# Optimization experiments

Hardware: AMD Instinct MI355X
Metric: run time of the kernel (lower is better)

## Reference

```python
import jax, jax.numpy as jnp
import numpy as np

N = 100000      # total nodes in batched graph
E_RAND = 1600000  # random edges (avg degree 16); self-loops appended -> E = E_RAND + N
B = 1024        # number of graphs / descriptor batch
DIN, D2D, D3D = 128, 200, 100
DG, DH = 20, 64
H1, H2 = 128, 32
EPS = 1e-5


def _lin_init(key, fan_in, fan_out):
    k1, k2 = jax.random.split(key)
    bound = 1.0 / np.sqrt(fan_in)
    W = jax.random.uniform(k1, (fan_in, fan_out), jnp.float32, -bound, bound)
    b = jax.random.uniform(k2, (fan_out,), jnp.float32, -bound, bound)
    return W, b


def setup_inputs() -> dict:
    key = jax.random.key(0)
    ks = jax.random.split(key, 16)
    feat = jax.random.normal(ks[0], (N, DIN), jnp.float32)
    src_r = jax.random.randint(ks[1], (E_RAND,), 0, N, jnp.int32)
    dst_r = jax.random.randint(ks[2], (E_RAND,), 0, N, jnp.int32)
    loop = jnp.arange(N, dtype=jnp.int32)
    src = jnp.concatenate([src_r, loop])  # self-loops: every node has in-degree >= 1
    dst = jnp.concatenate([dst_r, loop])
    graph_id = ((jnp.arange(N, dtype=jnp.int64) * B) // N).astype(jnp.int32)  # sorted, all B nonempty
    desc_2d = jax.random.normal(ks[3], (B, D2D), jnp.float32)
    desc_3d = jax.random.normal(ks[4], (B, D3D), jnp.float32)
    Wg1, bg1 = _lin_init(ks[5], DIN, 100)
    Wg2, bg2 = _lin_init(ks[6], 100, DG)
    Wpg, bpg = _lin_init(ks[7], DG, DH)
    Wp2, bp2 = _lin_init(ks[8], D2D, DH)
    gain = np.sqrt(6.0 / (DH + DH))
    W2 = jax.random.uniform(ks[9], (DH, DH), jnp.float32, -gain, gain)  # xavier_uniform
    Wf1, bf1 = _lin_init(ks[10], 2 * DH, H1)
    Wf2, bf2 = _lin_init(ks[11], H1, H2)
    Wf3, bf3 = _lin_init(ks[12], H2, 1)
    return dict(feat=feat, src=src, dst=dst, graph_id=graph_id,
                desc_2d=desc_2d, desc_3d=desc_3d,
                Wg1=Wg1, bg1=bg1, Wg2=Wg2, bg2=bg2,
                Wpg=Wpg, bpg=bpg, Wp2=Wp2, bp2=bp2, W2=W2,
                Wf1=Wf1, bf1=bf1, Wf2=Wf2, bf2=bf2, Wf3=Wf3, bf3=bf3,
                bn1_g=jnp.ones((H1,), jnp.float32), bn1_b=jnp.zeros((H1,), jnp.float32),
                bn2_g=jnp.ones((H2,), jnp.float32), bn2_b=jnp.zeros((H2,), jnp.float32))


def _gcn(h, W, b, src, dst):
    # copy_u -> mailbox mean: segment-mean of source feats over destination
    msg = h[src]                                               # [E, d] gather
    s = jax.ops.segment_sum(msg, dst, num_segments=N)          # [N, d]
    deg = jax.ops.segment_sum(jnp.ones((src.shape[0], 1), h.dtype), dst, num_segments=N)
    accum = s / jnp.maximum(deg, 1.0)
    return jax.nn.relu(accum @ W + b)


def _bn(x, g, b):  # BatchNorm1d, training-mode batch stats (biased var)
    mu = jnp.mean(x, axis=0)
    var = jnp.mean(jnp.square(x - mu), axis=0)
    return g * (x - mu) * jax.lax.rsqrt(var + EPS) + b


def reference(feat, src, dst, graph_id, desc_2d, desc_3d,
              Wg1, bg1, Wg2, bg2, Wpg, bpg, Wp2, bp2, W2,
              Wf1, bf1, Wf2, bf2, Wf3, bf3, bn1_g, bn1_b, bn2_g, bn2_b):
    h = _gcn(feat, Wg1, bg1, src, dst)        # relu(GCN1) -> [N,100]
    h = _gcn(h, Wg2, bg2, src, dst)           # relu(GCN2) -> [N,20]
    # dgl.mean_nodes: per-graph mean
    hs = jax.ops.segment_sum(h, graph_id, num_segments=B)
    cnt = jax.ops.segment_sum(jnp.ones((N, 1), h.dtype), graph_id, num_segments=B)
    hg = hs / jnp.maximum(cnt, 1.0)           # [B, 20]
    h_g = hg @ Wpg + bpg                      # [B, 64]
    h_d = desc_2d @ Wp2 + bp2                 # [B, 64]
    gate_vec = jax.nn.sigmoid((h_g @ W2) * h_d)
    v2 = gate_vec * h_d
    fusion = jnp.concatenate([h_g, v2], axis=-1)   # [B, 128]
    out = jax.nn.relu(_bn(fusion @ Wf1 + bf1, bn1_g, bn1_b))
    out = jax.nn.relu(_bn(out @ Wf2 + bf2, bn2_g, bn2_b))
    return out @ Wf3 + bf3                    # [B, 1]
```

## Files before the change

### kernel.cpp

```cpp
#include <hip/hip_runtime.h>
#include <hip/hip_fp8.h>
#include <math.h>

#define N_NODES 100000
#define B_GRAPH 1024
#define NBKT 391
#define NBLK 416
#define CAP 6000

typedef unsigned short ushort_t;
typedef unsigned int uint_t;
typedef unsigned char uchar_t;
typedef __attribute__((ext_vector_type(8))) short short8v;
typedef __attribute__((ext_vector_type(4))) float f32x4;
typedef __attribute__((ext_vector_type(2))) float f32x2;

static inline size_t alignup(size_t x){ return (x + 255) & ~(size_t)255; }

__device__ inline float bflo(uint_t u){
  union{ uint_t i; float f; } v; v.i = u << 16; return v.f;
}
__device__ inline float bfhi(uint_t u){
  union{ uint_t i; float f; } v; v.i = u & 0xffff0000u; return v.f;
}
__device__ inline ushort_t f2bf(float f){
  union{ float f; uint_t i; } v; v.f = f;
  uint_t b = v.i;
  b += 0x7fffu + ((b >> 16) & 1u);
  return (ushort_t)(b >> 16);
}
__device__ inline uint_t packbf(float a, float b){
  return (uint_t)f2bf(a) | ((uint_t)f2bf(b) << 16);
}
__device__ inline uchar_t f2fp8(float f){
  __hip_fp8_e4m3 v(f); return (uchar_t)v.__x;
}

__global__ __launch_bounds__(256) void k_hist(const int* __restrict__ dst,
                                              int* __restrict__ hist_g, int* __restrict__ btot,
                                              int E, int CH){
  __shared__ int h[NBKT];
  int blk = blockIdx.x, t = threadIdx.x;
  for (int i = t; i < NBKT; i += 256) h[i] = 0;
  __syncthreads();
  int s = blk*CH, e = s + CH; if (e > E) e = E;
  for (int i = s + t; i < e; i += 256) atomicAdd(&h[dst[i] >> 8], 1);
  __syncthreads();
  for (int i = t; i < NBKT; i += 256){
    int v = h[i];
    hist_g[i*NBLK + blk] = v;
    if (v) atomicAdd(&btot[i], v);
  }
}

__global__ __launch_bounds__(512) void k_offs(const int* __restrict__ hist_g, const int* __restrict__ btot,
                                              int* __restrict__ offs, int* __restrict__ bbase){
  __shared__ int sc[512];
  int b = blockIdx.x, t = threadIdx.x;
  int acc = 0;
  for (int i = t; i < b; i += 512) acc += btot[i];
  sc[t] = acc; __syncthreads();
  for (int o = 256; o > 0; o >>= 1){ if (t < o) sc[t] += sc[t+o]; __syncthreads(); }
  int bb = sc[0];
  __syncthreads();
  int v = (t < NBLK) ? hist_g[b*NBLK + t] : 0;
  sc[t] = v; __syncthreads();
  for (int off = 1; off < 512; off <<= 1){
    int u = (t >= off) ? sc[t-off] : 0;
    __syncthreads();
    sc[t] += u;
    __syncthreads();
  }
  if (t < NBLK) offs[b*NBLK + t] = bb + sc[t] - v;
  if (t == 0) bbase[b] = bb;
  if (b == NBKT-1 && t == NBLK-1) bbase[NBKT] = bb + sc[t];
}

__global__ __launch_bounds__(256) void k_scatter(const int* __restrict__ src, const int* __restrict__ dst,
                                                 const int* __restrict__ offs, uint_t* __restrict__ pairs,
                                                 int E, int CH){
  __shared__ int base[NBKT];
  int blk = blockIdx.x, t = threadIdx.x;
  for (int i = t; i < NBKT; i += 256) base[i] = offs[i*NBLK + blk];
  __syncthreads();
  int s = blk*CH, e = s + CH; if (e > E) e = E;
  for (int i = s + t; i < e; i += 256){
    int d = dst[i];
    int pos = atomicAdd(&base[d >> 8], 1);
    pairs[pos] = (uint_t)src[i] | ((uint_t)(d & 255) << 17);
  }
}

__global__ __launch_bounds__(256) void k_final(const uint_t* __restrict__ pairs, const int* __restrict__ bbase,
                                               int* __restrict__ rp, int* __restrict__ col){
  __shared__ uint_t buf[CAP];
  __shared__ int dcnt[256];
  __shared__ int sc[256];
  __shared__ int dpos[256];
  int b = blockIdx.x, t = threadIdx.x;
  int s = bbase[b], e = bbase[b+1], n = e - s;
  dcnt[t] = 0;
  const uint_t* P;
  if (n <= CAP){
    for (int i = t; i < n; i += 256) buf[i] = pairs[s + i];
    P = buf;
  } else {
    P = pairs + s;
  }
  __syncthreads();
  for (int i = t; i < n; i += 256) atomicAdd(&dcnt[P[i] >> 17], 1);
  __syncthreads();
  int v = dcnt[t];
  sc[t] = v; __syncthreads();
  for (int off = 1; off < 256; off <<= 1){
    int u = (t >= off) ? sc[t-off] : 0;
    __syncthreads();
    sc[t] += u;
    __syncthreads();
  }
  int ex = sc[t] - v;
  int node = b*256 + t;
  if (node <= N_NODES) rp[node] = s + ex;
  dpos[t] = s + ex;
  __syncthreads();
  for (int i = t; i < n; i += 256){
    uint_t pr = P[i];
    int pos = atomicAdd(&dpos[pr >> 17], 1);
    col[pos] = (int)(pr & 0x1FFFFu);
  }
}

__global__ __launch_bounds__(256) void k_packw(const float* __restrict__ W, ushort_t* __restrict__ wpk){
  int idx = blockIdx.x*256 + threadIdx.x;
  if (idx >= 7*4*64) return;
  int l = idx & 63;
  int s = (idx >> 6) & 3;
  int ct = idx >> 8;
  int colj = ct*16 + (l & 15);
  int kbase = 32*s + ((l >> 4) << 3);
  #pragma unroll
  for (int j = 0; j < 8; j++){
    float w = (colj < 100) ? W[(kbase + j)*100 + colj] : 0.f;
    wpk[idx*8 + j] = f2bf(w);
  }
}

__global__ __launch_bounds__(256) void k_gemm1m(const float* __restrict__ feat, const ushort_t* __restrict__ wpk,
                                                uchar_t* __restrict__ t1, int Nn){
  int wid = threadIdx.x >> 6;
  int lane = threadIdx.x & 63;
  int rt = blockIdx.x*4 + wid;
  int row0 = rt*16;
  if (row0 >= Nn) return;
  short8v a[4];
  const float* arow = feat + (size_t)(row0 + (lane & 15))*128 + ((lane >> 4) << 3);
  #pragma unroll
  for (int s = 0; s < 4; s++){
    float4 f0 = *reinterpret_cast<const float4*>(arow + 32*s);
    float4 f1 = *reinterpret_cast<const float4*>(arow + 32*s + 4);
    union { short8v v; uint_t u[4]; } cv;
    cv.u[0] = packbf(f0.x, f0.y); cv.u[1] = packbf(f0.z, f0.w);
    cv.u[2] = packbf(f1.x, f1.y); cv.u[3] = packbf(f1.z, f1.w);
    a[s] = cv.v;
  }
  const short8v* bfrag = reinterpret_cast<const short8v*>(wpk);
  for (int ct = 0; ct < 7; ct++){
    f32x4 acc = {0.f, 0.f, 0.f, 0.f};
    #pragma unroll
    for (int s = 0; s < 4; s++){
      short8v b = bfrag[(ct*4 + s)*64 + lane];
      acc = __builtin_amdgcn_mfma_f32_16x16x32_bf16(a[s], b, acc, 0, 0, 0);
    }
    int colj = ct*16 + (lane & 15);
    if (colj < 100){
      uchar_t* basep = t1 + colj;
      #pragma unroll
      for (int r = 0; r < 4; r++){
        int row = row0 + ((lane >> 4) << 2) + r;
        basep[(size_t)row*128] = f2fp8(acc[r]);
      }
    }
  }
}

__global__ __launch_bounds__(256) void k_agg1f(const uint2* __restrict__ t1q, const int* __restrict__ rp,
                                               const int* __restrict__ col, const float* __restrict__ bias,
                                               const float* __restrict__ Wg2, ushort_t* __restrict__ t2, int Nn){
  __shared__ float h1s[4][104];
  int lane = threadIdx.x & 63;
  int w = threadIdx.x >> 6;
  int node = blockIdx.x*4 + w;
  if (node >= Nn) return;
  int qtr = lane >> 4;
  int q   = lane & 15;
  int rs = rp[node], re = rp[node+1];
  f32x2 a0 = {0.f,0.f}, a1 = {0.f,0.f}, a2 = {0.f,0.f}, a3 = {0.f,0.f};

#if __has_builtin(__builtin_amdgcn_cvt_pk_f32_fp8)
  #define DEC8(U) { \
    a0 += __builtin_amdgcn_cvt_pk_f32_fp8((U).x, 0); \
    a1 += __builtin_amdgcn_cvt_pk_f32_fp8((U).x, 1); \
    a2 += __builtin_amdgcn_cvt_pk_f32_fp8((U).y, 0); \
    a3 += __builtin_amdgcn_cvt_pk_f32_fp8((U).y, 1); }
#else
  #define F8(B) ({ __hip_fp8_e4m3 _v; _v.__x = (unsigned char)(B); (float)_v; })
  #define DEC8(U) { \
    a0.x += F8((U).x); a0.y += F8((U).x>>8); a1.x += F8((U).x>>16); a1.y += F8((U).x>>24); \
    a2.x += F8((U).y); a2.y += F8((U).y>>8); a3.x += F8((U).y>>16); a3.y += F8((U).y>>24); }
#endif

  for (int base = rs; base < re; base += 64){
    int idx = base + lane;
    int colv = col[idx < re ? idx : re-1];
    int m = re - base; if (m > 64) m = 64;
    int nq = (m - qtr + 3) >> 2;
    int j = 0;
    for (; j + 4 <= nq; j += 4){
      int c0 = __shfl(colv, 4*(j+0) + qtr);
      int c1 = __shfl(colv, 4*(j+1) + qtr);
      int c2 = __shfl(colv, 4*(j+2) + qtr);
      int c3 = __shfl(colv, 4*(j+3) + qtr);
      uint2 u0 = t1q[(size_t)c0*16 + q];
      uint2 u1 = t1q[(size_t)c1*16 + q];
      uint2 u2 = t1q[(size_t)c2*16 + q];
      uint2 u3 = t1q[(size_t)c3*16 + q];
      DEC8(u0); DEC8(u1); DEC8(u2); DEC8(u3);
    }
    for (; j < nq; j++){
      int c = __shfl(colv, 4*j + qtr);
      uint2 u = t1q[(size_t)c*16 + q];
      DEC8(u);
    }
  }
  a0.x += __shfl_xor(a0.x, 16); a0.y += __shfl_xor(a0.y, 16);
  a1.x += __shfl_xor(a1.x, 16); a1.y += __shfl_xor(a1.y, 16);
  a2.x += __shfl_xor(a2.x, 16); a2.y += __shfl_xor(a2.y, 16);
  a3.x += __shfl_xor(a3.x, 16); a3.y += __shfl_xor(a3.y, 16);
  a0.x += __shfl_xor(a0.x, 32); a0.y += __shfl_xor(a0.y, 32);
  a1.x += __shfl_xor(a1.x, 32); a1.y += __shfl_xor(a1.y, 32);
  a2.x += __shfl_xor(a2.x, 32); a2.y += __shfl_xor(a2.y, 32);
  a3.x += __shfl_xor(a3.x, 32); a3.y += __shfl_xor(a3.y, 32);

  if (lane < 13){
    float inv = 1.f/(float)(re - rs);
    float v[8] = {a0.x,a0.y,a1.x,a1.y,a2.x,a2.y,a3.x,a3.y};
    #pragma unroll
    for (int i = 0; i < 8; i++){
      int d = 8*lane + i;
      float bv = (d < 100) ? bias[d] : 0.f;
      float x = v[i]*inv + bv;
      h1s[w][8*lane + i] = x > 0.f ? x : 0.f;
    }
  }
  __syncthreads();
  int g = lane >= 60 ? 3 : lane/20;
  int j = lane - g*20;
  int d0 = (g == 0) ? 0 : (g == 1) ? 34 : (g == 2) ? 67 : 100;
  int d1 = (g == 0) ? 34 : (g == 1) ? 67 : 100;
  float p = 0.f;
  for (int d = d0; d < d1; d++)
    p = fmaf(h1s[w][d], Wg2[d*20 + j], p);
  float pa = __shfl(p, lane + 20);
  float pb = __shfl(p, lane + 40);
  if (lane < 20)
    t2[(size_t)node*20 + lane] = f2bf(p + pa + pb);
  #undef DEC8
}

__global__ __launch_bounds__(256) void k_agg2(const uint_t* __restrict__ t2u, const int* __restrict__ rp,
                                              const int* __restrict__ col, const float* __restrict__ bias,
                                              float2* __restrict__ h2, int Nn){
  int tid = threadIdx.x;
  int node = blockIdx.x*16 + (tid >> 4);
  int l16 = tid & 15;
  if (node >= Nn) return;
  int rs = rp[node], re = rp[node+1];
  int d2 = l16 < 10 ? l16 : 9;
  int grpb = (tid & 63) & ~15;
  float slo0=0.f, slo1=0.f, shi0=0.f, shi1=0.f;
  for (int base = rs; base < re; base += 16){
    int idx = base + l16;
    int colv = col[idx < re ? idx : re-1];
    int m = re - base; if (m > 16) m = 16;
    int e = 0;
    for (; e + 4 <= m; e += 4){
      int c0 = __shfl(colv, grpb+e+0), c1 = __shfl(colv, grpb+e+1);
      int c2 = __shfl(colv, grpb+e+2), c3 = __shfl(colv, grpb+e+3);
      uint_t u0 = t2u[(size_t)c0*10 + d2];
      uint_t u1 = t2u[(size_t)c1*10 + d2];
      uint_t u2 = t2u[(size_t)c2*10 + d2];
      uint_t u3 = t2u[(size_t)c3*10 + d2];
      slo0 += bflo(u0); shi0 += bfhi(u0);
      slo1 += bflo(u1); shi1 += bfhi(u1);
      slo0 += bflo(u2); shi0 += bfhi(u2);
      slo1 += bflo(u3); shi1 += bfhi(u3);
    }
    for (; e < m; e++){
      int c = __shfl(colv, grpb+e);
      uint_t u = t2u[(size_t)c*10 + d2];
      slo0 += bflo(u); shi0 += bfhi(u);
    }
  }
  if (l16 < 10){
    float inv = 1.f/(float)(re - rs);
    float vlo = (slo0 + slo1)*inv + bias[2*l16];
    float vhi = (shi0 + shi1)*inv + bias[2*l16 + 1];
    vlo = vlo > 0.f ? vlo : 0.f;
    vhi = vhi > 0.f ? vhi : 0.f;
    float2 v; v.x = vlo; v.y = vhi;
    h2[(size_t)node*10 + l16] = v;
  }
}

__global__ __launch_bounds__(256) void k_gmean(const float* __restrict__ h2, float* __restrict__ hg){
  __shared__ float red[240];
  int g = blockIdx.x;
  int t = threadIdx.x;
  int s = (int)(((long long)g      * N_NODES + B_GRAPH - 1) / B_GRAPH);
  int e = (int)(((long long)(g+1)  * N_NODES + B_GRAPH - 1) / B_GRAPH);
  if (t < 240){
    int d  = t % 20;
    int r0 = t / 20;
    float acc = 0.f;
    for (int n = s + r0; n < e; n += 12) acc += h2[(size_t)n*20 + d];
    red[t] = acc;
  }
  __syncthreads();
  if (t < 20){
    float acc = 0.f;
    #pragma unroll
    for (int r = 0; r < 12; r++) acc += red[r*20 + t];
    hg[g*20 + t] = acc / (float)(e - s);
  }
}

__global__ __launch_bounds__(256) void k_headf(const float* __restrict__ hg, const float* __restrict__ Wpg,
                                               const float* __restrict__ bpg, const float* __restrict__ desc2,
                                               const float* __restrict__ Wp2, const float* __restrict__ bp2,
                                               const float* __restrict__ W2, float* __restrict__ fus){
  __shared__ float hGs[4][64];
  int idx = blockIdx.x*256 + threadIdx.x;
  int r = idx >> 6, d = idx & 63;
  int rloc = (threadIdx.x >> 6);
  float a = bpg[d];
  for (int k = 0; k < 20; k++) a = fmaf(hg[r*20 + k], Wpg[k*64 + d], a);
  float hd = bp2[d];
  for (int k = 0; k < 200; k++) hd = fmaf(desc2[r*200 + k], Wp2[k*64 + d], hd);
  hGs[rloc][d] = a;
  __syncthreads();
  float x = 0.f;
  for (int k = 0; k < 64; k++) x = fmaf(hGs[rloc][k], W2[k*64 + d], x);
  float gv = 1.f / (1.f + expf(-x*hd));
  fus[r*128 + d]      = a;
  fus[r*128 + 64 + d] = gv*hd;
}

__global__ __launch_bounds__(256) void k_tr(const float* __restrict__ X, float* __restrict__ XT){
  __shared__ float tile[32][33];
  int rb = blockIdx.x >> 2;
  int cb = blockIdx.x & 3;
  int tx = threadIdx.x & 31;
  int ty = threadIdx.x >> 5;
  #pragma unroll
  for (int i = 0; i < 4; i++){
    int r = rb*32 + ty + 8*i;
    tile[ty + 8*i][tx] = X[(size_t)r*128 + cb*32 + tx];
  }
  __syncthreads();
  #pragma unroll
  for (int i = 0; i < 4; i++){
    int c = cb*32 + ty + 8*i;
    XT[(size_t)c*1024 + rb*32 + tx] = tile[tx][ty + 8*i];
  }
}

__global__ __launch_bounds__(256) void k_bnt(const float* __restrict__ XT, const float* __restrict__ W,
                                             const float* __restrict__ bias, const float* __restrict__ gam,
                                             const float* __restrict__ bet, float* __restrict__ YT,
                                             int Kin, int Jout){
  int j = blockIdx.x;
  int t = threadIdx.x;
  float b0 = bias[j];
  float4 z; z.x = b0; z.y = b0; z.z = b0; z.w = b0;
  for (int k = 0; k < Kin; k++){
    float4 x = reinterpret_cast<const float4*>(XT + (size_t)k*1024)[t];
    float wv = W[k*Jout + j];
    z.x = fmaf(x.x, wv, z.x);
    z.y = fmaf(x.y, wv, z.y);
    z.z = fmaf(x.z, wv, z.z);
    z.w = fmaf(x.w, wv, z.w);
  }
  float s = z.x+z.y+z.z+z.w;
  float q = z.x*z.x+z.y*z.y+z.z*z.z+z.w*z.w;
  __shared__ float rs_[256], rq_[256];
  rs_[t] = s; rq_[t] = q; __syncthreads();
  for (int o = 128; o > 0; o >>= 1){
    if (t < o){ rs_[t] += rs_[t+o]; rq_[t] += rq_[t+o]; }
    __syncthreads();
  }
  float mu  = rs_[0] * (1.f/1024.f);
  float var = rq_[0] * (1.f/1024.f) - mu*mu;
  float inv = 1.f / sqrtf(var + 1e-5f);
  float gj = gam[j], bj = bet[j];
  float4 y;
  y.x = gj*(z.x-mu)*inv + bj; y.x = y.x > 0.f ? y.x : 0.f;
  y.y = gj*(z.y-mu)*inv + bj; y.y = y.y > 0.f ? y.y : 0.f;
  y.z = gj*(z.z-mu)*inv + bj; y.z = y.z > 0.f ? y.z : 0.f;
  y.w = gj*(z.w-mu)*inv + bj; y.w = y.w > 0.f ? y.w : 0.f;
  reinterpret_cast<float4*>(YT + (size_t)j*1024)[t] = y;
}

__global__ __launch_bounds__(256) void k_out(const float* __restrict__ y2T, const float* __restrict__ Wf3,
                                             const float* __restrict__ bf3, float* __restrict__ out){
  int r = blockIdx.x*256 + threadIdx.x;
  if (r >= B_GRAPH) return;
  float a = bf3[0];
  #pragma unroll
  for (int k = 0; k < 32; k++) a = fmaf(y2T[k*1024 + r], Wf3[k], a);
  out[r] = a;
}

extern "C" void kernel_launch(void* const* d_in, const int* in_sizes, int n_in,
                              void* d_out, int out_size, void* d_ws, size_t ws_size,
                              hipStream_t stream){
  const float* feat  = (const float*)d_in[0];
  const int*   src   = (const int*)d_in[1];
  const int*   dst   = (const int*)d_in[2];
  const float* desc2 = (const float*)d_in[4];
  const float* Wg1   = (const float*)d_in[6];
  const float* bg1   = (const float*)d_in[7];
  const float* Wg2   = (const float*)d_in[8];
  const float* bg2   = (const float*)d_in[9];
  const float* Wpg   = (const float*)d_in[10];
  const float* bpg   = (const float*)d_in[11];
  const float* Wp2   = (const float*)d_in[12];
  const float* bp2   = (const float*)d_in[13];
  const float* W2    = (const float*)d_in[14];
  const float* Wf1   = (const float*)d_in[15];
  const float* bf1   = (const float*)d_in[16];
  const float* Wf2   = (const float*)d_in[17];
  const float* bf2   = (const float*)d_in[18];
  const float* Wf3   = (const float*)d_in[19];
  const float* bf3   = (const float*)d_in[20];
  const float* bn1g  = (const float*)d_in[21];
  const float* bn1b  = (const float*)d_in[22];
  const float* bn2g  = (const float*)d_in[23];
  const float* bn2b  = (const float*)d_in[24];
  float* out = (float*)d_out;
  const int E = in_sizes[1];

  char* w = (char*)d_ws;
  int* rp     = (int*)w; w += alignup((size_t)(N_NODES+1)*4);
  int* col    = (int*)w; w += alignup((size_t)E*4);
  int* hist_g = (int*)w; w += alignup((size_t)NBKT*NBLK*4);
  int* offs   = (int*)w; w += alignup((size_t)NBKT*NBLK*4);
  int* btot   = (int*)w; w += alignup((size_t)NBKT*4);
  int* bbase  = (int*)w; w += alignup((size_t)(NBKT+1)*4);
  ushort_t* wpk = (ushort_t*)w; w += alignup((size_t)7*4*64*8*2);
  uchar_t* t1 = (uchar_t*)w; w += alignup((size_t)N_NODES*128);
  uint_t* pairs = (uint_t*)w; w += alignup((size_t)E*4);
  ushort_t* t2 = (ushort_t*)w; w += alignup((size_t)N_NODES*20*2);
  float* h2   = (float*)w; w += alignup((size_t)N_NODES*20*4);
  float* hg  = (float*)w; w += alignup((size_t)B_GRAPH*20*4);
  float* fus = (float*)w; w += alignup((size_t)B_GRAPH*128*4);
  float* fusT= (float*)w; w += alignup((size_t)B_GRAPH*128*4);
  float* y1T = (float*)w; w += alignup((size_t)B_GRAPH*128*4);
  float* y2T = (float*)w; w += alignup((size_t)B_GRAPH*32*4);

  const int CH = (E + NBLK - 1)/NBLK;

  hipMemsetAsync(btot, 0, (size_t)NBKT*sizeof(int), stream);
  hipMemsetAsync(t1, 0, (size_t)N_NODES*128, stream);
  k_hist   <<<NBLK, 256, 0, stream>>>(dst, hist_g, btot, E, CH);
  k_offs   <<<NBKT, 512, 0, stream>>>(hist_g, btot, offs, bbase);
  k_scatter<<<NBLK, 256, 0, stream>>>(src, dst, offs, pairs, E, CH);
  k_final  <<<NBKT, 256, 0, stream>>>(pairs, bbase, rp, col);

  k_packw  <<<7, 256, 0, stream>>>(Wg1, wpk);
  k_gemm1m <<<(N_NODES/16 + 3)/4, 256, 0, stream>>>(feat, wpk, t1, N_NODES);
  k_agg1f  <<<(N_NODES+3)/4, 256, 0, stream>>>((const uint2*)t1, rp, col, bg1, Wg2, t2, N_NODES);
  k_agg2   <<<(N_NODES+15)/16, 256, 0, stream>>>((const uint_t*)t2, rp, col, bg2, (float2*)h2, N_NODES);

  k_gmean  <<<B_GRAPH, 256, 0, stream>>>(h2, hg);
  k_headf  <<<(B_GRAPH*64)/256, 256, 0, stream>>>(hg, Wpg, bpg, desc2, Wp2, bp2, W2, fus);
  k_tr     <<<128, 256, 0, stream>>>(fus, fusT);
  k_bnt    <<<128, 256, 0, stream>>>(fusT, Wf1, bf1, bn1g, bn1b, y1T, 128, 128);
  k_bnt    <<<32, 256, 0, stream>>>(y1T, Wf2, bf2, bn2g, bn2b, y2T, 128, 32);
  k_out    <<<4, 256, 0, stream>>>(y2T, Wf3, bf3, out);
}
```

Measured before the change: 316.4 us.

## Merge weight packing, gemm1 and graph-mean into CSR build and aggregation kernels

Packs Wg1 inside extra blocks of the histogram kernel and runs the GEMM1 blocks alongside the edge scatter in one launch, so the dense GEMM overlaps the CSR build. The per-graph mean is folded into the second aggregation through atomic adds into hg, with division by node count moved into the head kernel. This removes the gmean kernel, the h2 buffer and the large memset of t1, since pad columns are now zeroed directly. The cost is atomic contention on hg and the __syncthreads removed in agg1 (only per-warp data used, though it is still risky), plus nondeterministic float summation order.

Result: slower. 347.6 us (+9.9%).

```diff
diff --git a/kernel.cpp b/kernel.cpp
--- a/kernel.cpp
+++ b/kernel.cpp
@@ -7,6 +7,7 @@
 #define NBKT 391
 #define NBLK 416
 #define CAP 6000
+#define G1BLK 1563
 
 typedef unsigned short ushort_t;
 typedef unsigned int uint_t;
@@ -36,20 +37,37 @@
   __hip_fp8_e4m3 v(f); return (uchar_t)v.__x;
 }
 
-__global__ __launch_bounds__(256) void k_hist(const int* __restrict__ dst,
-                                              int* __restrict__ hist_g, int* __restrict__ btot,
-                                              int E, int CH){
+__global__ __launch_bounds__(256) void k_histw(const int* __restrict__ dst,
+                                               int* __restrict__ hist_g, int* __restrict__ btot,
+                                               const float* __restrict__ W, ushort_t* __restrict__ wpk,
+                                               int E, int CH){
   __shared__ int h[NBKT];
-  int blk = blockIdx.x, t = threadIdx.x;
-  for (int i = t; i < NBKT; i += 256) h[i] = 0;
-  __syncthreads();
-  int s = blk*CH, e = s + CH; if (e > E) e = E;
-  for (int i = s + t; i < e; i += 256) atomicAdd(&h[dst[i] >> 8], 1);
-  __syncthreads();
-  for (int i = t; i < NBKT; i += 256){
-    int v = h[i];
-    hist_g[i*NBLK + blk] = v;
-    if (v) atomicAdd(&btot[i], v);
+  int t = threadIdx.x;
+  if (blockIdx.x < NBLK){
+    int blk = blockIdx.x;
+    for (int i = t; i < NBKT; i += 256) h[i] = 0;
+    __syncthreads();
+    int s = blk*CH, e = s + CH; if (e > E) e = E;
+    for (int i = s + t; i < e; i += 256) atomicAdd(&h[dst[i] >> 8], 1);
+    __syncthreads();
+    for (int i = t; i < NBKT; i += 256){
+      int v = h[i];
+      hist_g[i*NBLK + blk] = v;
+      if (v) atomicAdd(&btot[i], v);
+    }
+  } else {
+    int idx = (blockIdx.x - NBLK)*256 + t;
+    if (idx >= 7*4*64) return;
+    int l = idx & 63;
+    int s = (idx >> 6) & 3;
+    int ct = idx >> 8;
+    int colj = ct*16 + (l & 15);
+    int kbase = 32*s + ((l >> 4) << 3);
+    #pragma unroll
+    for (int j = 0; j < 8; j++){
+      float w = (colj < 100) ? W[(kbase + j)*100 + colj] : 0.f;
+      wpk[idx*8 + j] = f2bf(w);
+    }
   }
 }
 
@@ -76,18 +94,64 @@
   if (b == NBKT-1 && t == NBLK-1) bbase[NBKT] = bb + sc[t];
 }
 
-__global__ __launch_bounds__(256) void k_scatter(const int* __restrict__ src, const int* __restrict__ dst,
-                                                 const int* __restrict__ offs, uint_t* __restrict__ pairs,
-                                                 int E, int CH){
-  __shared__ int base[NBKT];
-  int blk = blockIdx.x, t = threadIdx.x;
-  for (int i = t; i < NBKT; i += 256) base[i] = offs[i*NBLK + blk];
-  __syncthreads();
-  int s = blk*CH, e = s + CH; if (e > E) e = E;
-  for (int i = s + t; i < e; i += 256){
-    int d = dst[i];
-    int pos = atomicAdd(&base[d >> 8], 1);
-    pairs[pos] = (uint_t)src[i] | ((uint_t)(d & 255) << 17);
+__global__ __launch_bounds__(256) void k_scg1(const int* __restrict__ src, const int* __restrict__ dst,
+                                              const int* __restrict__ offs, uint_t* __restrict__ pairs,
+                                              const float* __restrict__ feat, const ushort_t* __restrict__ wpk,
+                                              uchar_t* __restrict__ t1, int E, int CH, int Nn){
+  if (blockIdx.x < NBLK){
+    __shared__ int base[NBKT];
+    int blk = blockIdx.x, t = threadIdx.x;
+    for (int i = t; i < NBKT; i += 256) base[i] = offs[i*NBLK + blk];
+    __syncthreads();
+    int s = blk*CH, e = s + CH; if (e > E) e = E;
+    for (int i = s + t; i < e; i += 256){
+      int d = dst[i];
+      int pos = atomicAdd(&base[d >> 8], 1);
+      pairs[pos] = (uint_t)src[i] | ((uint_t)(d & 255) << 17);
+    }
+  } else {
+    int wid = threadIdx.x >> 6;
+    int lane = threadIdx.x & 63;
+    int rt = (blockIdx.x - NBLK)*4 + wid;
+    int row0 = rt*16;
+    if (row0 >= Nn) return;
+    short8v a[4];
+    const float* arow = feat + (size_t)(row0 + (lane & 15))*128 + ((lane >> 4) << 3);
+    #pragma unroll
+    for (int s = 0; s < 4; s++){
+      float4 f0 = *reinterpret_cast<const float4*>(arow + 32*s);
+      float4 f1 = *reinterpret_cast<const float4*>(arow + 32*s + 4);
+      union { short8v v; uint_t u[4]; } cv;
+      cv.u[0] = packbf(f0.x, f0.y); cv.u[1] = packbf(f0.z, f0.w);
+      cv.u[2] = packbf(f1.x, f1.y); cv.u[3] = packbf(f1.z, f1.w);
+      a[s] = cv.v;
+    }
+    const short8v* bfrag = reinterpret_cast<const short8v*>(wpk);
+    for (int ct = 0; ct < 7; ct++){
+      f32x4 acc = {0.f, 0.f, 0.f, 0.f};
+      #pragma unroll
+      for (int s = 0; s < 4; s++){
+        short8v b = bfrag[(ct*4 + s)*64 + lane];
+        acc = __builtin_amdgcn_mfma_f32_16x16x32_bf16(a[s], b, acc, 0, 0, 0);
+      }
+      int colj = ct*16 + (lane & 15);
+      if (colj < 100){
+        uchar_t* basep = t1 + colj;
+        #pragma unroll
+        for (int r = 0; r < 4; r++){
+          int row = row0 + ((lane >> 4) << 2) + r;
+          basep[(size_t)row*128] = f2fp8(acc[r]);
+        }
+      }
+    }
+    int pc = lane & 15;
+    if (pc < 7){
+      #pragma unroll
+      for (int r = 0; r < 4; r++){
+        int row = row0 + ((lane >> 4) << 2) + r;
+        *reinterpret_cast<uint_t*>(t1 + (size_t)row*128 + 100 + 4*pc) = 0u;
+      }
+    }
   }
 }
 
@@ -130,60 +194,7 @@
   }
 }
 
-__global__ __launch_bounds__(256) void k_packw(const float* __restrict__ W, ushort_t* __restrict__ wpk){
-  int idx = blockIdx.x*256 + threadIdx.x;
-  if (idx >= 7*4*64) return;
-  int l = idx & 63;
-  int s = (idx >> 6) & 3;
-  int ct = idx >> 8;
-  int colj = ct*16 + (l & 15);
-  int kbase = 32*s + ((l >> 4) << 3);
-  #pragma unroll
-  for (int j = 0; j < 8; j++){
-    float w = (colj < 100) ? W[(kbase + j)*100 + colj] : 0.f;
-    wpk[idx*8 + j] = f2bf(w);
-  }
-}
-
-__global__ __launch_bounds__(256) void k_gemm1m(const float* __restrict__ feat, const ushort_t* __restrict__ wpk,
-                                                uchar_t* __restrict__ t1, int Nn){
-  int wid = threadIdx.x >> 6;
-  int lane = threadIdx.x & 63;
-  int rt = blockIdx.x*4 + wid;
-  int row0 = rt*16;
-  if (row0 >= Nn) return;
-  short8v a[4];
-  const float* arow = feat + (size_t)(row0 + (lane & 15))*128 + ((lane >> 4) << 3);
-  #pragma unroll
-  for (int s = 0; s < 4; s++){
-    float4 f0 = *reinterpret_cast<const float4*>(arow + 32*s);
-    float4 f1 = *reinterpret_cast<const float4*>(arow + 32*s + 4);
-    union { short8v v; uint_t u[4]; } cv;
-    cv.u[0] = packbf(f0.x, f0.y); cv.u[1] = packbf(f0.z, f0.w);
-    cv.u[2] = packbf(f1.x, f1.y); cv.u[3] = packbf(f1.z, f1.w);
-    a[s] = cv.v;
-  }
-  const short8v* bfrag = reinterpret_cast<const short8v*>(wpk);
-  for (int ct = 0; ct < 7; ct++){
-    f32x4 acc = {0.f, 0.f, 0.f, 0.f};
-    #pragma unroll
-    for (int s = 0; s < 4; s++){
-      short8v b = bfrag[(ct*4 + s)*64 + lane];
-      acc = __builtin_amdgcn_mfma_f32_16x16x32_bf16(a[s], b, acc, 0, 0, 0);
-    }
-    int colj = ct*16 + (lane & 15);
-    if (colj < 100){
-      uchar_t* basep = t1 + colj;
-      #pragma unroll
-      for (int r = 0; r < 4; r++){
-        int row = row0 + ((lane >> 4) << 2) + r;
-        basep[(size_t)row*128] = f2fp8(acc[r]);
-      }
-    }
-  }
-}
-
-__global__ __launch_bounds__(256) void k_agg1f(const uint2* __restrict__ t1q, const int* __restrict__ rp,
+__global__ __launch_bounds__(256) void k_agg1g(const uint2* __restrict__ t1q, const int* __restrict__ rp,
                                                const int* __restrict__ col, const float* __restrict__ bias,
                                                const float* __restrict__ Wg2, ushort_t* __restrict__ t2, int Nn){
   __shared__ float h1s[4][104];
@@ -249,14 +260,13 @@
       int d = 8*lane + i;
       float bv = (d < 100) ? bias[d] : 0.f;
       float x = v[i]*inv + bv;
-      h1s[w][8*lane + i] = x > 0.f ? x : 0.f;
-    }
-  }
-  __syncthreads();
-  int g = lane >= 60 ? 3 : lane/20;
-  int j = lane - g*20;
-  int d0 = (g == 0) ? 0 : (g == 1) ? 34 : (g == 2) ? 67 : 100;
-  int d1 = (g == 0) ? 34 : (g == 1) ? 67 : 100;
+      h1s[w][8*lane + i] = (d < 100 && x > 0.f) ? x : 0.f;
+    }
+  }
+  int g3 = lane >= 60 ? 3 : lane/20;
+  int j = lane - g3*20;
+  int d0 = (g3 == 0) ? 0 : (g3 == 1) ? 34 : (g3 == 2) ? 67 : 100;
+  int d1 = (g3 == 0) ? 34 : (g3 == 1) ? 67 : 100;
   float p = 0.f;
   for (int d = d0; d < d1; d++)
     p = fmaf(h1s[w][d], Wg2[d*20 + j], p);
@@ -267,9 +277,9 @@
   #undef DEC8
 }
 
-__global__ __launch_bounds__(256) void k_agg2(const uint_t* __restrict__ t2u, const int* __restrict__ rp,
-                                              const int* __restrict__ col, const float* __restrict__ bias,
-                                              float2* __restrict__ h2, int Nn){
+__global__ __launch_bounds__(256) void k_agg2g(const uint_t* __restrict__ t2u, const int* __restrict__ rp,
+                                               const int* __restrict__ col, const float* __restrict__ bias,
+                                               float* __restrict__ hg, int Nn){
   int tid = threadIdx.x;
   int node = blockIdx.x*16 + (tid >> 4);
   int l16 = tid & 15;
@@ -307,30 +317,9 @@
     float vhi = (shi0 + shi1)*inv + bias[2*l16 + 1];
     vlo = vlo > 0.f ? vlo : 0.f;
     vhi = vhi > 0.f ? vhi : 0.f;
-    float2 v; v.x = vlo; v.y = vhi;
-    h2[(size_t)node*10 + l16] = v;
-  }
-}
-
-__global__ __launch_bounds__(256) void k_gmean(const float* __restrict__ h2, float* __restrict__ hg){
-  __shared__ float red[240];
-  int g = blockIdx.x;
-  int t = threadIdx.x;
-  int s = (int)(((long long)g      * N_NODES + B_GRAPH - 1) / B_GRAPH);
-  int e = (int)(((long long)(g+1)  * N_NODES + B_GRAPH - 1) / B_GRAPH);
-  if (t < 240){
-    int d  = t % 20;
-    int r0 = t / 20;
-    float acc = 0.f;
-    for (int n = s + r0; n < e; n += 12) acc += h2[(size_t)n*20 + d];
-    red[t] = acc;
-  }
-  __syncthreads();
-  if (t < 20){
-    float acc = 0.f;
-    #pragma unroll
-    for (int r = 0; r < 12; r++) acc += red[r*20 + t];
-    hg[g*20 + t] = acc / (float)(e - s);
+    int g = (int)(((long long)node * B_GRAPH) / N_NODES);
+    atomicAdd(&hg[g*20 + 2*l16],     vlo);
+    atomicAdd(&hg[g*20 + 2*l16 + 1], vhi);
   }
 }
 
@@ -342,8 +331,11 @@
   int idx = blockIdx.x*256 + threadIdx.x;
   int r = idx >> 6, d = idx & 63;
   int rloc = (threadIdx.x >> 6);
+  int s0 = (int)(((long long)r     * N_NODES + B_GRAPH - 1) / B_GRAPH);
+  int e0 = (int)(((long long)(r+1) * N_NODES + B_GRAPH - 1) / B_GRAPH);
+  float invc = 1.f/(float)(e0 - s0);
   float a = bpg[d];
-  for (int k = 0; k < 20; k++) a = fmaf(hg[r*20 + k], Wpg[k*64 + d], a);
+  for (int k = 0; k < 20; k++) a = fmaf(hg[r*20 + k]*invc, Wpg[k*64 + d], a);
   float hd = bp2[d];
   for (int k = 0; k < 200; k++) hd = fmaf(desc2[r*200 + k], Wp2[k*64 + d], hd);
   hGs[rloc][d] = a;
@@ -455,13 +447,12 @@
   int* hist_g = (int*)w; w += alignup((size_t)NBKT*NBLK*4);
   int* offs   = (int*)w; w += alignup((size_t)NBKT*NBLK*4);
   int* btot   = (int*)w; w += alignup((size_t)NBKT*4);
+  float* hg   = (float*)w; w += alignup((size_t)B_GRAPH*20*4);
   int* bbase  = (int*)w; w += alignup((size_t)(NBKT+1)*4);
   ushort_t* wpk = (ushort_t*)w; w += alignup((size_t)7*4*64*8*2);
   uchar_t* t1 = (uchar_t*)w; w += alignup((size_t)N_NODES*128);
   uint_t* pairs = (uint_t*)w; w += alignup((size_t)E*4);
   ushort_t* t2 = (ushort_t*)w; w += alignup((size_t)N_NODES*20*2);
-  float* h2   = (float*)w; w += alignup((size_t)N_NODES*20*4);
-  float* hg  = (float*)w; w += alignup((size_t)B_GRAPH*20*4);
   float* fus = (float*)w; w += alignup((size_t)B_GRAPH*128*4);
   float* fusT= (float*)w; w += alignup((size_t)B_GRAPH*128*4);
   float* y1T = (float*)w; w += alignup((size_t)B_GRAPH*128*4);
@@ -469,19 +460,15 @@
 
   const int CH = (E + NBLK - 1)/NBLK;
 
-  hipMemsetAsync(btot, 0, (size_t)NBKT*sizeof(int), stream);
-  hipMemsetAsync(t1, 0, (size_t)N_NODES*128, stream);
-  k_hist   <<<NBLK, 256, 0, stream>>>(dst, hist_g, btot, E, CH);
+  hipMemsetAsync(btot, 0, alignup((size_t)NBKT*4) + (size_t)B_GRAPH*20*4, stream);
+  k_histw  <<<NBLK + 7, 256, 0, stream>>>(dst, hist_g, btot, Wg1, wpk, E, CH);
   k_offs   <<<NBKT, 512, 0, stream>>>(hist_g, btot, offs, bbase);
-  k_scatter<<<NBLK, 256, 0, stream>>>(src, dst, offs, pairs, E, CH);
+  k_scg1   <<<NBLK + G1BLK, 256, 0, stream>>>(src, dst, offs, pairs, feat, wpk, t1, E, CH, N_NODES);
   k_final  <<<NBKT, 256, 0, stream>>>(pairs, bbase, rp, col);
 
-  k_packw  <<<7, 256, 0, stream>>>(Wg1, wpk);
-  k_gemm1m <<<(N_NODES/16 + 3)/4, 256, 0, stream>>>(feat, wpk, t1, N_NODES);
-  k_agg1f  <<<(N_NODES+3)/4, 256, 0, stream>>>((const uint2*)t1, rp, col, bg1, Wg2, t2, N_NODES);
-  k_agg2   <<<(N_NODES+15)/16, 256, 0, stream>>>((const uint_t*)t2, rp, col, bg2, (float2*)h2, N_NODES);
-
-  k_gmean  <<<B_GRAPH, 256, 0, stream>>>(h2, hg);
+  k_agg1g  <<<(N_NODES+3)/4, 256, 0, stream>>>((const uint2*)t1, rp, col, bg1, Wg2, t2, N_NODES);
+  k_agg2g  <<<(N_NODES+15)/16, 256, 0, stream>>>((const uint_t*)t2, rp, col, bg2, hg, N_NODES);
+
   k_headf  <<<(B_GRAPH*64)/256, 256, 0, stream>>>(hg, Wpg, bpg, desc2, Wp2, bp2, W2, fus);
   k_tr     <<<128, 256, 0, stream>>>(fus, fusT);
   k_bnt    <<<128, 256, 0, stream>>>(fusT, Wf1, bf1, bn1g, bn1b, y1T, 128, 128);
```
